# Kernel optimization log

Measured on AMD Instinct MI355X. Metric: run time of the kernel, lower is better.

## Reference

```python
import jax, jax.numpy as jnp
import numpy as np

N_NODES = 100000
N_EDGES = 3200000
D_IN = 256
D_OUT = 256


def setup_inputs() -> dict:
    key = jax.random.key(0)
    k1, k2, k3, k4, k5, k6 = jax.random.split(key, 6)
    x = jax.random.normal(k1, (N_NODES, D_IN), dtype=jnp.float32)
    edge_row = jax.random.randint(k2, (N_EDGES,), 0, N_NODES, dtype=jnp.int32)
    edge_col = jax.random.randint(k3, (N_EDGES,), 0, N_NODES, dtype=jnp.int32)
    edge_val = jax.random.uniform(k4, (N_EDGES,), dtype=jnp.float32)
    # nn.Linear params (PyTorch stores weight as [out, in]; we apply x @ W.T + b)
    bound = 1.0 / np.sqrt(D_IN)
    W = jax.random.uniform(k5, (D_OUT, D_IN), minval=-bound, maxval=bound, dtype=jnp.float32)
    b = jax.random.uniform(k6, (D_OUT,), minval=-bound, maxval=bound, dtype=jnp.float32)
    return {"x": x, "edge_row": edge_row, "edge_col": edge_col,
            "edge_val": edge_val, "W": W, "b": b}


def reference(x, edge_row, edge_col, edge_val, W, b):
    # SpMM: agg[i] = sum over edges e with row[e]==i of val[e] * x[col[e]]
    messages = edge_val[:, None] * x[edge_col]          # [E, D_in]
    agg = jax.ops.segment_sum(messages, edge_row, num_segments=N_NODES)  # [N, D_in]
    # Dense linear: agg @ W.T + b
    return jnp.einsum('nd,od->no', agg, W) + b
```

## Files before the change

### kernel.cpp

```cpp
#include <hip/hip_runtime.h>

#define THREADS 256

typedef __attribute__((ext_vector_type(8))) short short8;
typedef __attribute__((ext_vector_type(4))) float f32x4;

__device__ __forceinline__ unsigned short f2bf(float f) {
    unsigned u = __builtin_bit_cast(unsigned, f);
    return (unsigned short)((u + 0x7FFFu + ((u >> 16) & 1u)) >> 16);
}
__device__ __forceinline__ float bf2f_lo(unsigned u) { return __builtin_bit_cast(float, u << 16); }
__device__ __forceinline__ float bf2f_hi(unsigned u) { return __builtin_bit_cast(float, u & 0xFFFF0000u); }


__global__ void init_gcur512(int* __restrict__ gcur, int capB) {
    int i = blockIdx.x * blockDim.x + threadIdx.x;
    if (i < 512) gcur[i] = i * capB;
}

__global__ void p1_sort(const int* __restrict__ row, const int* __restrict__ col,
                        const float* __restrict__ val, int* __restrict__ gcur,
                        uint2* __restrict__ estage, int n_edges, int nbkt, int capB) {
    __shared__ int h[512];
    __shared__ int curl[512];
    int tid = threadIdx.x, bid = blockIdx.x;
    int E0 = (int)((long long)bid * n_edges / gridDim.x);
    int E1 = (int)((long long)(bid + 1) * n_edges / gridDim.x);
    for (int i = tid; i < 512; i += THREADS) h[i] = 0;
    __syncthreads();
    for (int e = E0 + tid; e < E1; e += THREADS)
        atomicAdd(&h[row[e] >> 8], 1);
    __syncthreads();
    for (int b = tid; b < nbkt; b += THREADS) {
        int c = h[b];
        curl[b] = c ? atomicAdd(&gcur[b], c) : 0;
    }
    __syncthreads();
    for (int e = E0 + tid; e < E1; e += THREADS) {
        int r = row[e];
        int b = r >> 8;
        int pos = atomicAdd(&curl[b], 1);
        if (pos < (b + 1) * capB)
            estage[pos] = make_uint2(((unsigned)(r & 255) << 24) | (unsigned)col[e],
                                     (unsigned)__float_as_int(val[e]));
    }
}

__global__ void bcnt_kernel(const int* __restrict__ gcur, int* __restrict__ bcnt,
                            int capB, int nbkt) {
    int i = blockIdx.x * blockDim.x + threadIdx.x;
    if (i < nbkt) {
        int c = gcur[i] - i * capB;
        bcnt[i] = c > capB ? capB : c;
    }
}

__global__ void bscan_kernel(const int* __restrict__ cnt, int* __restrict__ offs,
                             int* __restrict__ cur, int n) {
    __shared__ int buf[2][THREADS];
    __shared__ int running_s;
    int tid = threadIdx.x;
    if (tid == 0) running_s = 0;
    __syncthreads();
    for (int base = 0; base < n; base += THREADS) {
        int idx = base + tid;
        int v = (idx < n) ? cnt[idx] : 0;
        int incl = v;
        int cb = 0;
        buf[0][tid] = incl;
        __syncthreads();
        #pragma unroll
        for (int off = 1; off < THREADS; off <<= 1) {
            int t = incl;
            if (tid >= off) t += buf[cb][tid - off];
            cb ^= 1;
            buf[cb][tid] = t;
            incl = t;
            __syncthreads();
        }
        int base_run = running_s;
        if (idx < n) {
            int excl = base_run + incl - v;
            offs[idx] = excl;
            cur[idx] = excl;
        }
        int total = buf[cb][THREADS - 1];
        __syncthreads();
        if (tid == 0) running_s = base_run + total;
        __syncthreads();
    }
    if (tid == 0) offs[n] = running_s;
}

__global__ void p2_sort(const uint2* __restrict__ estage, const int* __restrict__ gcur,
                        const int* __restrict__ bbase, int2* __restrict__ pr,
                        int* __restrict__ offs, int capB, int n_nodes, int n_edges,
                        int nbkt) {
    __shared__ int h[256];
    __shared__ int curh[256];
    __shared__ int wsum[4];
    int b = blockIdx.x, tid = threadIdx.x;
    int base = b * capB;
    int count = gcur[b] - base; if (count > capB) count = capB;
    h[tid] = 0;
    __syncthreads();
    for (int i = tid; i < count; i += THREADS)
        atomicAdd(&h[estage[base + i].x >> 24], 1);
    __syncthreads();
    int v = h[tid];
    int lane = tid & 63, w = tid >> 6;
    int incl = v;
    #pragma unroll
    for (int off = 1; off < 64; off <<= 1) {
        int t = __shfl_up(incl, off, 64);
        if (lane >= off) incl += t;
    }
    if (lane == 63) wsum[w] = incl;
    __syncthreads();
    int wo = 0;
    for (int i = 0; i < w; ++i) wo += wsum[i];
    int excl = wo + incl - v;
    int gb = bbase[b];
    int node = b * 256 + tid;
    if (node < n_nodes) offs[node] = gb + excl;
    curh[tid] = gb + excl;
    if (b == nbkt - 1 && tid == 0) offs[n_nodes] = n_edges;
    __syncthreads();
    for (int i = tid; i < count; i += THREADS) {
        uint2 p = estage[base + i];
        int q = atomicAdd(&curh[(int)(p.x >> 24)], 1);
        pr[q] = make_int2((int)(p.x & 0x00FFFFFFu), (int)p.y);
    }
}


__global__ void zero_kernel(int* __restrict__ p, int n) {
    int i = blockIdx.x * blockDim.x + threadIdx.x;
    if (i < n) p[i] = 0;
}

__global__ void hist_part_kernel(const int* __restrict__ row, int* __restrict__ cnt,
                                 int n_edges, int n_nodes) {
    int g = blockIdx.x & 7;
    int inst = blockIdx.x >> 3;
    int ninst = gridDim.x >> 3;
    int lo = (int)(((long long)g * n_nodes) >> 3);
    int hi = (int)(((long long)(g + 1) * n_nodes) >> 3);
    int e0 = (int)(((long long)inst * n_edges) / ninst);
    int e1 = (int)(((long long)(inst + 1) * n_edges) / ninst);
    for (int e = e0 + threadIdx.x; e < e1; e += THREADS) {
        int r = row[e];
        if (r >= lo && r < hi) atomicAdd(&cnt[r], 1);
    }
}

__global__ void place_part_kernel(const int* __restrict__ row, const int* __restrict__ col,
                                  const float* __restrict__ val, int* __restrict__ cur,
                                  int2* __restrict__ pr, int n_edges, int n_nodes) {
    int g = blockIdx.x & 7;
    int inst = blockIdx.x >> 3;
    int ninst = gridDim.x >> 3;
    int lo = (int)(((long long)g * n_nodes) >> 3);
    int hi = (int)(((long long)(g + 1) * n_nodes) >> 3);
    int e0 = (int)(((long long)inst * n_edges) / ninst);
    int e1 = (int)(((long long)(inst + 1) * n_edges) / ninst);
    for (int e = e0 + threadIdx.x; e < e1; e += THREADS) {
        int r = row[e];
        if (r >= lo && r < hi) {
            int p = atomicAdd(&cur[r], 1);
            pr[p] = make_int2(col[e], __float_as_int(val[e]));
        }
    }
}

__global__ void scan1_kernel(const int* __restrict__ cnt, int* __restrict__ offs,
                             int* __restrict__ bsum, int n) {
    int tid = threadIdx.x;
    int base = blockIdx.x * 1024 + tid * 4;
    int v0 = 0, v1 = 0, v2 = 0, v3 = 0;
    if (base + 3 < n) {
        int4 v = *reinterpret_cast<const int4*>(cnt + base);
        v0 = v.x; v1 = v.y; v2 = v.z; v3 = v.w;
    } else {
        if (base + 0 < n) v0 = cnt[base + 0];
        if (base + 1 < n) v1 = cnt[base + 1];
        if (base + 2 < n) v2 = cnt[base + 2];
    }
    int ts = v0 + v1 + v2 + v3;
    int lane = tid & 63;
    int incl = ts;
    #pragma unroll
    for (int off = 1; off < 64; off <<= 1) {
        int t = __shfl_up(incl, off, 64);
        if (lane >= off) incl += t;
    }
    __shared__ int wsum[4];
    int w = tid >> 6;
    if (lane == 63) wsum[w] = incl;
    __syncthreads();
    int wo = 0;
    for (int i = 0; i < w; ++i) wo += wsum[i];
    int excl = wo + incl - ts;
    if (base + 0 < n) offs[base + 0] = excl;
    if (base + 1 < n) offs[base + 1] = excl + v0;
    if (base + 2 < n) offs[base + 2] = excl + v0 + v1;
    if (base + 3 < n) offs[base + 3] = excl + v0 + v1 + v2;
    if (tid == THREADS - 1) bsum[blockIdx.x] = wo + incl;
}

__global__ void scan2_kernel(int* __restrict__ bsum, int nb) {
    int tid = threadIdx.x;
    int base = tid * 4;
    int v0 = 0, v1 = 0, v2 = 0, v3 = 0;
    if (base + 0 < nb) v0 = bsum[base + 0];
    if (base + 1 < nb) v1 = bsum[base + 1];
    if (base + 2 < nb) v2 = bsum[base + 2];
    if (base + 3 < nb) v3 = bsum[base + 3];
    int ts = v0 + v1 + v2 + v3;
    int lane = tid & 63;
    int incl = ts;
    #pragma unroll
    for (int off = 1; off < 64; off <<= 1) {
        int t = __shfl_up(incl, off, 64);
        if (lane >= off) incl += t;
    }
    __shared__ int wsum[4];
    int w = tid >> 6;
    if (lane == 63) wsum[w] = incl;
    __syncthreads();
    int wo = 0;
    for (int i = 0; i < w; ++i) wo += wsum[i];
    int excl = wo + incl - ts;
    if (base + 0 < nb) bsum[base + 0] = excl;
    if (base + 1 < nb) bsum[base + 1] = excl + v0;
    if (base + 2 < nb) bsum[base + 2] = excl + v0 + v1;
    if (base + 3 < nb) bsum[base + 3] = excl + v0 + v1 + v2;
    if (tid == THREADS - 1) bsum[nb] = wo + incl;
}

__global__ void scan3_kernel(int* __restrict__ offs, const int* __restrict__ bsum,
                             int* __restrict__ cur, int n) {
    int i = blockIdx.x * blockDim.x + threadIdx.x;
    if (i < n) {
        int v = offs[i] + bsum[i >> 10];
        offs[i] = v;
        cur[i] = v;
    }
    if (i == 0) offs[n] = bsum[(n + 1023) >> 10];
}


__global__ void cvt_bf16_kernel(const float4* __restrict__ in, uint4* __restrict__ out, int n8) {
    int i = blockIdx.x * blockDim.x + threadIdx.x;
    if (i >= n8) return;
    float4 a = in[2 * i], b = in[2 * i + 1];
    uint4 o;
    o.x = (unsigned)f2bf(a.x) | ((unsigned)f2bf(a.y) << 16);
    o.y = (unsigned)f2bf(a.z) | ((unsigned)f2bf(a.w) << 16);
    o.z = (unsigned)f2bf(b.x) | ((unsigned)f2bf(b.y) << 16);
    o.w = (unsigned)f2bf(b.z) | ((unsigned)f2bf(b.w) << 16);
    out[i] = o;
}

__global__ void cvt_W_pack_kernel(const float* __restrict__ W, unsigned short* __restrict__ WbP) {
    int f = blockIdx.x * blockDim.x + threadIdx.x;
    if (f >= 8192) return;
    int l = f & 63, nt = (f >> 6) & 15, k0i = f >> 10;
    int r = nt * 16 + (l & 15);
    int koff = k0i * 32 + 8 * (l >> 4);
    const float4* s = reinterpret_cast<const float4*>(W + r * 256 + koff);
    float4 a = s[0], b = s[1];
    uint4 o;
    o.x = (unsigned)f2bf(a.x) | ((unsigned)f2bf(a.y) << 16);
    o.y = (unsigned)f2bf(a.z) | ((unsigned)f2bf(a.w) << 16);
    o.z = (unsigned)f2bf(b.x) | ((unsigned)f2bf(b.y) << 16);
    o.w = (unsigned)f2bf(b.z) | ((unsigned)f2bf(b.w) << 16);
    reinterpret_cast<uint4*>(WbP)[f] = o;
}

template<int OUT_BF16>
__global__ void spmm_bf16_kernel(const uint2* __restrict__ xb, const int* __restrict__ offs,
                                 const int2* __restrict__ pr, void* __restrict__ outp,
                                 int nnodes) {
    int wid = (blockIdx.x * blockDim.x + threadIdx.x) >> 6;
    int lane = threadIdx.x & 63;
    if (wid >= nnodes) return;
    int s = offs[wid], e = offs[wid + 1];
    float a0 = 0.f, a1 = 0.f, a2 = 0.f, a3 = 0.f;
    int i = s;
    if (i < e && (i & 1)) {
        int2 p = pr[i];
        uint2 xv = xb[(size_t)p.x * 64 + lane];
        float v = __int_as_float(p.y);
        a0 = fmaf(v, bf2f_lo(xv.x), a0); a1 = fmaf(v, bf2f_hi(xv.x), a1);
        a2 = fmaf(v, bf2f_lo(xv.y), a2); a3 = fmaf(v, bf2f_hi(xv.y), a3);
        ++i;
    }
    for (; i + 8 <= e; i += 8) {
        int4 pa = *reinterpret_cast<const int4*>(pr + i);
        int4 pb = *reinterpret_cast<const int4*>(pr + i + 2);
        int4 pc = *reinterpret_cast<const int4*>(pr + i + 4);
        int4 pd = *reinterpret_cast<const int4*>(pr + i + 6);
        uint2 x0 = xb[(size_t)pa.x * 64 + lane];
        uint2 x1 = xb[(size_t)pa.z * 64 + lane];
        uint2 x2 = xb[(size_t)pb.x * 64 + lane];
        uint2 x3 = xb[(size_t)pb.z * 64 + lane];
        uint2 x4_ = xb[(size_t)pc.x * 64 + lane];
        uint2 x5 = xb[(size_t)pc.z * 64 + lane];
        uint2 x6 = xb[(size_t)pd.x * 64 + lane];
        uint2 x7 = xb[(size_t)pd.z * 64 + lane];
        float v0 = __int_as_float(pa.y), v1 = __int_as_float(pa.w);
        float v2 = __int_as_float(pb.y), v3 = __int_as_float(pb.w);
        float v4 = __int_as_float(pc.y), v5 = __int_as_float(pc.w);
        float v6 = __int_as_float(pd.y), v7 = __int_as_float(pd.w);
        a0 = fmaf(v0, bf2f_lo(x0.x), a0); a1 = fmaf(v0, bf2f_hi(x0.x), a1);
        a2 = fmaf(v0, bf2f_lo(x0.y), a2); a3 = fmaf(v0, bf2f_hi(x0.y), a3);
        a0 = fmaf(v1, bf2f_lo(x1.x), a0); a1 = fmaf(v1, bf2f_hi(x1.x), a1);
        a2 = fmaf(v1, bf2f_lo(x1.y), a2); a3 = fmaf(v1, bf2f_hi(x1.y), a3);
        a0 = fmaf(v2, bf2f_lo(x2.x), a0); a1 = fmaf(v2, bf2f_hi(x2.x), a1);
        a2 = fmaf(v2, bf2f_lo(x2.y), a2); a3 = fmaf(v2, bf2f_hi(x2.y), a3);
        a0 = fmaf(v3, bf2f_lo(x3.x), a0); a1 = fmaf(v3, bf2f_hi(x3.x), a1);
        a2 = fmaf(v3, bf2f_lo(x3.y), a2); a3 = fmaf(v3, bf2f_hi(x3.y), a3);
        a0 = fmaf(v4, bf2f_lo(x4_.x), a0); a1 = fmaf(v4, bf2f_hi(x4_.x), a1);
        a2 = fmaf(v4, bf2f_lo(x4_.y), a2); a3 = fmaf(v4, bf2f_hi(x4_.y), a3);
        a0 = fmaf(v5, bf2f_lo(x5.x), a0); a1 = fmaf(v5, bf2f_hi(x5.x), a1);
        a2 = fmaf(v5, bf2f_lo(x5.y), a2); a3 = fmaf(v5, bf2f_hi(x5.y), a3);
        a0 = fmaf(v6, bf2f_lo(x6.x), a0); a1 = fmaf(v6, bf2f_hi(x6.x), a1);
        a2 = fmaf(v6, bf2f_lo(x6.y), a2); a3 = fmaf(v6, bf2f_hi(x6.y), a3);
        a0 = fmaf(v7, bf2f_lo(x7.x), a0); a1 = fmaf(v7, bf2f_hi(x7.x), a1);
        a2 = fmaf(v7, bf2f_lo(x7.y), a2); a3 = fmaf(v7, bf2f_hi(x7.y), a3);
    }
    for (; i + 2 <= e; i += 2) {
        int4 pa = *reinterpret_cast<const int4*>(pr + i);
        uint2 x0 = xb[(size_t)pa.x * 64 + lane];
        uint2 x1 = xb[(size_t)pa.z * 64 + lane];
        float v0 = __int_as_float(pa.y), v1 = __int_as_float(pa.w);
        a0 = fmaf(v0, bf2f_lo(x0.x), a0); a1 = fmaf(v0, bf2f_hi(x0.x), a1);
        a2 = fmaf(v0, bf2f_lo(x0.y), a2); a3 = fmaf(v0, bf2f_hi(x0.y), a3);
        a0 = fmaf(v1, bf2f_lo(x1.x), a0); a1 = fmaf(v1, bf2f_hi(x1.x), a1);
        a2 = fmaf(v1, bf2f_lo(x1.y), a2); a3 = fmaf(v1, bf2f_hi(x1.y), a3);
    }
    for (; i < e; ++i) {
        int2 p = pr[i];
        uint2 xv = xb[(size_t)p.x * 64 + lane];
        float v = __int_as_float(p.y);
        a0 = fmaf(v, bf2f_lo(xv.x), a0); a1 = fmaf(v, bf2f_hi(xv.x), a1);
        a2 = fmaf(v, bf2f_lo(xv.y), a2); a3 = fmaf(v, bf2f_hi(xv.y), a3);
    }
    if (OUT_BF16) {
        ushort4 o;
        o.x = f2bf(a0); o.y = f2bf(a1); o.z = f2bf(a2); o.w = f2bf(a3);
        *reinterpret_cast<ushort4*>((unsigned short*)outp + (size_t)wid * 256 + 4 * lane) = o;
    } else {
        ((float4*)outp)[(size_t)wid * 64 + lane] = make_float4(a0, a1, a2, a3);
    }
}

__global__ void spmm_f32_kernel(const float4* __restrict__ x4, const int* __restrict__ offs,
                                const int2* __restrict__ pr, float4* __restrict__ out4,
                                int nnodes) {
    int wid = (blockIdx.x * blockDim.x + threadIdx.x) >> 6;
    int lane = threadIdx.x & 63;
    if (wid >= nnodes) return;
    int s = offs[wid], e = offs[wid + 1];
    float4 acc = make_float4(0.f, 0.f, 0.f, 0.f);
    for (int i = s; i < e; ++i) {
        int2 p = pr[i];
        float4 xv = x4[(size_t)p.x * 64 + lane];
        float v = __int_as_float(p.y);
        acc.x = fmaf(v, xv.x, acc.x); acc.y = fmaf(v, xv.y, acc.y);
        acc.z = fmaf(v, xv.z, acc.z); acc.w = fmaf(v, xv.w, acc.w);
    }
    out4[(size_t)wid * 64 + lane] = acc;
}

__launch_bounds__(256)
__global__ void gemm_direct_kernel(const unsigned short* __restrict__ aggb,
                                   const unsigned short* __restrict__ WbP,
                                   const float* __restrict__ bias,
                                   float* __restrict__ out, int n) {
    int tid = threadIdx.x, lane = tid & 63, w = tid >> 6;
    int row0 = blockIdx.x * 64 + w * 16;
    int lr = lane & 15, lg = lane >> 4;
    const unsigned short* arow = aggb + (size_t)(row0 + lr) * 256 + lg * 8;
    short8 af[8];
    #pragma unroll
    for (int k = 0; k < 8; ++k)
        af[k] = *reinterpret_cast<const short8*>(arow + k * 32);
    f32x4 acc[16];
    #pragma unroll
    for (int nt = 0; nt < 16; ++nt) acc[nt] = (f32x4){0.f, 0.f, 0.f, 0.f};
    #pragma unroll
    for (int k = 0; k < 8; ++k) {
        #pragma unroll
        for (int nt = 0; nt < 16; ++nt) {
            short8 bf_ = *reinterpret_cast<const short8*>(
                &WbP[(size_t)((k * 16 + nt) * 64 + lane) * 8]);
            acc[nt] = __builtin_amdgcn_mfma_f32_16x16x32_bf16(af[k], bf_, acc[nt], 0, 0, 0);
        }
    }
    #pragma unroll
    for (int nt = 0; nt < 16; ++nt) {
        int gc = nt * 16 + lr;
        float bv = bias[gc];
        #pragma unroll
        for (int q = 0; q < 4; ++q) {
            int gr = row0 + lg * 4 + q;
            if (gr < n) out[(size_t)gr * 256 + gc] = acc[nt][q] + bv;
        }
    }
}

__launch_bounds__(256, 2)
__global__ void gemm_mfma_kernel(float* __restrict__ out, const unsigned short* __restrict__ Wb,
                                 const float* __restrict__ bias, int nrows) {
    __shared__ unsigned short As[64][264];
    __shared__ unsigned short Ws[256][40];
    int tid = threadIdx.x;
    int rowBase = blockIdx.x * 64;

    const float4* o4 = reinterpret_cast<const float4*>(out);
    for (int it = tid; it < 64 * 64; it += 256) {
        int r = it >> 6, c = it & 63;
        float4 v = make_float4(0.f, 0.f, 0.f, 0.f);
        int gr = rowBase + r;
        if (gr < nrows) v = o4[(size_t)gr * 64 + c];
        ushort4 w;
        w.x = f2bf(v.x); w.y = f2bf(v.y); w.z = f2bf(v.z); w.w = f2bf(v.w);
        *reinterpret_cast<ushort4*>(&As[r][c * 4]) = w;
    }

    int w = tid >> 6, lane = tid & 63;
    int lr = lane & 15, lg = lane >> 4;
    f32x4 acc[16];
    #pragma unroll
    for (int nt = 0; nt < 16; ++nt) acc[nt] = (f32x4){0.f, 0.f, 0.f, 0.f};

    for (int k0 = 0; k0 < 256; k0 += 32) {
        __syncthreads();
        for (int it = tid; it < 1024; it += 256) {
            int r = it >> 2, c = it & 3;
            uint4 v = *reinterpret_cast<const uint4*>(Wb + (size_t)r * 256 + k0 + c * 8);
            *reinterpret_cast<uint4*>(&Ws[r][c * 8]) = v;
        }
        __syncthreads();
        short8 af = *reinterpret_cast<const short8*>(&As[w * 16 + lr][k0 + 8 * lg]);
        #pragma unroll
        for (int nt = 0; nt < 16; ++nt) {
            short8 bf_ = *reinterpret_cast<const short8*>(&Ws[nt * 16 + lr][8 * lg]);
            acc[nt] = __builtin_amdgcn_mfma_f32_16x16x32_bf16(af, bf_, acc[nt], 0, 0, 0);
        }
    }

    #pragma unroll
    for (int nt = 0; nt < 16; ++nt) {
        int gc = nt * 16 + lr;
        float bv = bias[gc];
        #pragma unroll
        for (int q = 0; q < 4; ++q) {
            int gr = rowBase + w * 16 + lg * 4 + q;
            if (gr < nrows) out[(size_t)gr * 256 + gc] = acc[nt][q] + bv;
        }
    }
}


extern "C" void kernel_launch(void* const* d_in, const int* in_sizes, int n_in,
                              void* d_out, int out_size, void* d_ws, size_t ws_size,
                              hipStream_t stream) {
    const float* x     = (const float*)d_in[0];
    const int*   erow  = (const int*)d_in[1];
    const int*   ecol  = (const int*)d_in[2];
    const float* evalv = (const float*)d_in[3];
    const float* W     = (const float*)d_in[4];
    const float* bias  = (const float*)d_in[5];
    float* out = (float*)d_out;

    int n_nodes = in_sizes[0] / 256;
    int n_edges = in_sizes[1];

    int nbkt = (n_nodes + 255) >> 8;
    int avg = n_edges / (nbkt > 0 ? nbkt : 1);
    int capB = avg + avg / 4 + 1024;

    size_t A = (size_t)((n_nodes + 63) & ~63) + 64;
    int* offs  = (int*)d_ws;
    int* gcur  = offs + A;
    int* bcnt_ = gcur + 512;
    int* bbase = bcnt_ + 512;
    int* bscr  = bbase + 576;
    unsigned short* Wb  = (unsigned short*)(bscr + 512);
    unsigned short* WbP = Wb + 65536;
    int2* pr = (int2*)(WbP + 65536);
    int* after_pr = (int*)(pr + n_edges);

    size_t est_ints  = (size_t)nbkt * capB * 2;
    size_t aggb_ints = (size_t)n_nodes * 128;
    size_t xb_ints   = (size_t)n_nodes * 128;
    size_t alias_ints = est_ints > aggb_ints ? est_ints : aggb_ints;
    size_t head_ints = (size_t)(after_pr - (int*)d_ws);
    size_t need_new = (head_ints + alias_ints + xb_ints) * 4;
    bool new_ok = (nbkt <= 512) && (nbkt >= 1) && ws_size >= need_new;

    if (new_ok) {
        uint2* estage = (uint2*)after_pr;
        unsigned short* aggb = (unsigned short*)after_pr;
        unsigned short* xb = (unsigned short*)(after_pr + alias_ints);

        init_gcur512<<<2, THREADS, 0, stream>>>(gcur, capB);
        p1_sort<<<512, THREADS, 0, stream>>>(erow, ecol, evalv, gcur, estage,
                                             n_edges, nbkt, capB);
        bcnt_kernel<<<2, THREADS, 0, stream>>>(gcur, bcnt_, capB, nbkt);
        bscan_kernel<<<1, THREADS, 0, stream>>>(bcnt_, bbase, bscr, nbkt);
        p2_sort<<<nbkt, THREADS, 0, stream>>>(estage, gcur, bbase, pr, offs,
                                              capB, n_nodes, n_edges, nbkt);

        cvt_W_pack_kernel<<<32, THREADS, 0, stream>>>(W, WbP);
        int n8 = n_nodes * 32;
        cvt_bf16_kernel<<<(n8 + THREADS - 1) / THREADS, THREADS, 0, stream>>>(
            (const float4*)x, (uint4*)xb, n8);

        int spmm_blocks = (n_nodes + 3) / 4;
        spmm_bf16_kernel<1><<<spmm_blocks, THREADS, 0, stream>>>(
            (const uint2*)xb, offs, pr, aggb, n_nodes);
        int gb = (n_nodes + 63) / 64;
        gemm_direct_kernel<<<gb, THREADS, 0, stream>>>(aggb, WbP, bias, out, n_nodes);
    } else {
        int nb = (n_nodes + 1023) >> 10;
        size_t Af = (size_t)((n_nodes + 63) & ~63);
        int* cnt   = (int*)d_ws;
        int* offsf = cnt + Af;
        int* cur   = offsf + Af;
        int* bsum  = cur + Af;
        int* wbase = bsum + (((size_t)nb + 64) & ~63ull);
        unsigned short* Wbf = (unsigned short*)wbase;
        int2* prf  = (int2*)(Wbf + 65536);
        int* aft   = (int*)(prf + n_edges);
        unsigned short* xbf = (unsigned short*)aft;
        size_t need_old = (size_t)((char*)(xbf + (size_t)n_nodes * 256) - (char*)d_ws);
        bool told = ws_size >= need_old;

        zero_kernel<<<(n_nodes + THREADS - 1) / THREADS, THREADS, 0, stream>>>(cnt, n_nodes);
        hist_part_kernel<<<2048, THREADS, 0, stream>>>(erow, cnt, n_edges, n_nodes);
        scan1_kernel<<<nb, THREADS, 0, stream>>>(cnt, offsf, bsum, n_nodes);
        scan2_kernel<<<1, THREADS, 0, stream>>>(bsum, nb);
        scan3_kernel<<<(n_nodes + THREADS - 1) / THREADS, THREADS, 0, stream>>>(offsf, bsum, cur, n_nodes);
        place_part_kernel<<<2048, THREADS, 0, stream>>>(erow, ecol, evalv, cur, prf, n_edges, n_nodes);
        cvt_bf16_kernel<<<32, THREADS, 0, stream>>>((const float4*)W, (uint4*)Wbf, 65536 / 8);

        int gb = (n_nodes + 63) / 64;
        if (told) {
            int n8 = n_nodes * 32;
            cvt_bf16_kernel<<<(n8 + THREADS - 1) / THREADS, THREADS, 0, stream>>>(
                (const float4*)x, (uint4*)xbf, n8);
            int spmm_blocks = (n_nodes + 3) / 4;
            spmm_bf16_kernel<0><<<spmm_blocks, THREADS, 0, stream>>>(
                (const uint2*)xbf, offsf, prf, out, n_nodes);
        } else {
            int spmm_blocks = (n_nodes + 3) / 4;
            spmm_f32_kernel<<<spmm_blocks, THREADS, 0, stream>>>(
                (const float4*)x, offsf, prf, (float4*)out, n_nodes);
        }
        gemm_mfma_kernel<<<gb, THREADS, 0, stream>>>(out, Wbf, bias, n_nodes);
    }
}
```

Before: 439.5 us.

## Fuse bucket sort, W and x conversions into one launch; drop scan kernels; widen GEMM tile

Merges the first-pass bucket sort, the W bf16 packing and the x bf16 conversion into a single launch split by block index, and raises the sort-pass block count. The separate bucket-count and scan kernels are removed: gcur now holds relative counts, cleared by a memset, and each p2_sort block computes its own base offset by reducing the counts of earlier buckets. The GEMM now gives each wave 32 rows with two accumulator sets so that each loaded W fragment feeds two MFMAs. This trades several small serial launches for redundant per-block reductions and higher register pressure in the GEMM.

Result: slower. 455.6 us (+3.7%).

```diff
diff --git a/kernel.cpp b/kernel.cpp
--- a/kernel.cpp
+++ b/kernel.cpp
@@ -12,96 +12,89 @@
 __device__ __forceinline__ float bf2f_lo(unsigned u) { return __builtin_bit_cast(float, u << 16); }
 __device__ __forceinline__ float bf2f_hi(unsigned u) { return __builtin_bit_cast(float, u & 0xFFFF0000u); }
 
-
-__global__ void init_gcur512(int* __restrict__ gcur, int capB) {
-    int i = blockIdx.x * blockDim.x + threadIdx.x;
-    if (i < 512) gcur[i] = i * capB;
-}
-
-__global__ void p1_sort(const int* __restrict__ row, const int* __restrict__ col,
-                        const float* __restrict__ val, int* __restrict__ gcur,
-                        uint2* __restrict__ estage, int n_edges, int nbkt, int capB) {
-    __shared__ int h[512];
-    __shared__ int curl[512];
-    int tid = threadIdx.x, bid = blockIdx.x;
-    int E0 = (int)((long long)bid * n_edges / gridDim.x);
-    int E1 = (int)((long long)(bid + 1) * n_edges / gridDim.x);
-    for (int i = tid; i < 512; i += THREADS) h[i] = 0;
-    __syncthreads();
-    for (int e = E0 + tid; e < E1; e += THREADS)
-        atomicAdd(&h[row[e] >> 8], 1);
-    __syncthreads();
-    for (int b = tid; b < nbkt; b += THREADS) {
-        int c = h[b];
-        curl[b] = c ? atomicAdd(&gcur[b], c) : 0;
-    }
-    __syncthreads();
-    for (int e = E0 + tid; e < E1; e += THREADS) {
-        int r = row[e];
-        int b = r >> 8;
-        int pos = atomicAdd(&curl[b], 1);
-        if (pos < (b + 1) * capB)
-            estage[pos] = make_uint2(((unsigned)(r & 255) << 24) | (unsigned)col[e],
-                                     (unsigned)__float_as_int(val[e]));
-    }
-}
-
-__global__ void bcnt_kernel(const int* __restrict__ gcur, int* __restrict__ bcnt,
-                            int capB, int nbkt) {
-    int i = blockIdx.x * blockDim.x + threadIdx.x;
-    if (i < nbkt) {
-        int c = gcur[i] - i * capB;
-        bcnt[i] = c > capB ? capB : c;
-    }
-}
-
-__global__ void bscan_kernel(const int* __restrict__ cnt, int* __restrict__ offs,
-                             int* __restrict__ cur, int n) {
-    __shared__ int buf[2][THREADS];
-    __shared__ int running_s;
-    int tid = threadIdx.x;
-    if (tid == 0) running_s = 0;
-    __syncthreads();
-    for (int base = 0; base < n; base += THREADS) {
-        int idx = base + tid;
-        int v = (idx < n) ? cnt[idx] : 0;
-        int incl = v;
-        int cb = 0;
-        buf[0][tid] = incl;
+#define P1B 1024
+
+__global__ void fusedA_kernel(const int* __restrict__ row, const int* __restrict__ col,
+                              const float* __restrict__ val, int* __restrict__ gcur,
+                              uint2* __restrict__ estage,
+                              const float* __restrict__ W, unsigned short* __restrict__ WbP,
+                              const float4* __restrict__ x, uint4* __restrict__ xb,
+                              int n_edges, int nbkt, int capB, int n8) {
+    int b = blockIdx.x, tid = threadIdx.x;
+    if (b < P1B) {
+        __shared__ int h[512];
+        __shared__ int curl[512];
+        int E0 = (int)((long long)b * n_edges / P1B);
+        int E1 = (int)((long long)(b + 1) * n_edges / P1B);
+        for (int i = tid; i < 512; i += THREADS) h[i] = 0;
         __syncthreads();
-        #pragma unroll
-        for (int off = 1; off < THREADS; off <<= 1) {
-            int t = incl;
-            if (tid >= off) t += buf[cb][tid - off];
-            cb ^= 1;
-            buf[cb][tid] = t;
-            incl = t;
-            __syncthreads();
-        }
-        int base_run = running_s;
-        if (idx < n) {
-            int excl = base_run + incl - v;
-            offs[idx] = excl;
-            cur[idx] = excl;
-        }
-        int total = buf[cb][THREADS - 1];
+        for (int e = E0 + tid; e < E1; e += THREADS)
+            atomicAdd(&h[row[e] >> 8], 1);
         __syncthreads();
-        if (tid == 0) running_s = base_run + total;
+        for (int bk = tid; bk < nbkt; bk += THREADS) {
+            int c = h[bk];
+            curl[bk] = bk * capB + (c ? atomicAdd(&gcur[bk], c) : 0);
+        }
         __syncthreads();
-    }
-    if (tid == 0) offs[n] = running_s;
+        for (int e = E0 + tid; e < E1; e += THREADS) {
+            int r = row[e];
+            int bk = r >> 8;
+            int pos = atomicAdd(&curl[bk], 1);
+            if (pos < (bk + 1) * capB)
+                estage[pos] = make_uint2(((unsigned)(r & 255) << 24) | (unsigned)col[e],
+                                         (unsigned)__float_as_int(val[e]));
+        }
+    } else if (b < P1B + 32) {
+        int f = (b - P1B) * THREADS + tid;
+        int l = f & 63, nt = (f >> 6) & 15, k0i = f >> 10;
+        int r = nt * 16 + (l & 15);
+        int koff = k0i * 32 + 8 * (l >> 4);
+        const float4* s = reinterpret_cast<const float4*>(W + r * 256 + koff);
+        float4 a = s[0], bb = s[1];
+        uint4 o;
+        o.x = (unsigned)f2bf(a.x) | ((unsigned)f2bf(a.y) << 16);
+        o.y = (unsigned)f2bf(a.z) | ((unsigned)f2bf(a.w) << 16);
+        o.z = (unsigned)f2bf(bb.x) | ((unsigned)f2bf(bb.y) << 16);
+        o.w = (unsigned)f2bf(bb.z) | ((unsigned)f2bf(bb.w) << 16);
+        reinterpret_cast<uint4*>(WbP)[f] = o;
+    } else {
+        int i = (b - P1B - 32) * THREADS + tid;
+        if (i >= n8) return;
+        float4 a = x[2 * i], bb = x[2 * i + 1];
+        uint4 o;
+        o.x = (unsigned)f2bf(a.x) | ((unsigned)f2bf(a.y) << 16);
+        o.y = (unsigned)f2bf(a.z) | ((unsigned)f2bf(a.w) << 16);
+        o.z = (unsigned)f2bf(bb.x) | ((unsigned)f2bf(bb.y) << 16);
+        o.w = (unsigned)f2bf(bb.z) | ((unsigned)f2bf(bb.w) << 16);
+        reinterpret_cast<uint4*>(xb)[i] = o;
+    }
 }
 
 __global__ void p2_sort(const uint2* __restrict__ estage, const int* __restrict__ gcur,
-                        const int* __restrict__ bbase, int2* __restrict__ pr,
-                        int* __restrict__ offs, int capB, int n_nodes, int n_edges,
-                        int nbkt) {
+                        int2* __restrict__ pr, int* __restrict__ offs,
+                        int capB, int n_nodes, int nbkt) {
+    __shared__ int red[256];
     __shared__ int h[256];
     __shared__ int curh[256];
     __shared__ int wsum[4];
     int b = blockIdx.x, tid = threadIdx.x;
+
+    int partial = 0;
+    for (int j = tid; j < b; j += THREADS) {
+        int c = gcur[j];
+        partial += c > capB ? capB : c;
+    }
+    red[tid] = partial;
+    __syncthreads();
+    #pragma unroll
+    for (int s = 128; s > 0; s >>= 1) {
+        if (tid < s) red[tid] += red[tid + s];
+        __syncthreads();
+    }
+    int gb = red[0];
+    int count = gcur[b]; if (count > capB) count = capB;
     int base = b * capB;
-    int count = gcur[b] - base; if (count > capB) count = capB;
+
     h[tid] = 0;
     __syncthreads();
     for (int i = tid; i < count; i += THREADS)
@@ -120,162 +113,16 @@
     int wo = 0;
     for (int i = 0; i < w; ++i) wo += wsum[i];
     int excl = wo + incl - v;
-    int gb = bbase[b];
     int node = b * 256 + tid;
     if (node < n_nodes) offs[node] = gb + excl;
     curh[tid] = gb + excl;
-    if (b == nbkt - 1 && tid == 0) offs[n_nodes] = n_edges;
+    if (b == nbkt - 1 && tid == 0) offs[n_nodes] = gb + count;
     __syncthreads();
     for (int i = tid; i < count; i += THREADS) {
         uint2 p = estage[base + i];
         int q = atomicAdd(&curh[(int)(p.x >> 24)], 1);
         pr[q] = make_int2((int)(p.x & 0x00FFFFFFu), (int)p.y);
     }
-}
-
-
-__global__ void zero_kernel(int* __restrict__ p, int n) {
-    int i = blockIdx.x * blockDim.x + threadIdx.x;
-    if (i < n) p[i] = 0;
-}
-
-__global__ void hist_part_kernel(const int* __restrict__ row, int* __restrict__ cnt,
-                                 int n_edges, int n_nodes) {
-    int g = blockIdx.x & 7;
-    int inst = blockIdx.x >> 3;
-    int ninst = gridDim.x >> 3;
-    int lo = (int)(((long long)g * n_nodes) >> 3);
-    int hi = (int)(((long long)(g + 1) * n_nodes) >> 3);
-    int e0 = (int)(((long long)inst * n_edges) / ninst);
-    int e1 = (int)(((long long)(inst + 1) * n_edges) / ninst);
-    for (int e = e0 + threadIdx.x; e < e1; e += THREADS) {
-        int r = row[e];
-        if (r >= lo && r < hi) atomicAdd(&cnt[r], 1);
-    }
-}
-
-__global__ void place_part_kernel(const int* __restrict__ row, const int* __restrict__ col,
-                                  const float* __restrict__ val, int* __restrict__ cur,
-                                  int2* __restrict__ pr, int n_edges, int n_nodes) {
-    int g = blockIdx.x & 7;
-    int inst = blockIdx.x >> 3;
-    int ninst = gridDim.x >> 3;
-    int lo = (int)(((long long)g * n_nodes) >> 3);
-    int hi = (int)(((long long)(g + 1) * n_nodes) >> 3);
-    int e0 = (int)(((long long)inst * n_edges) / ninst);
-    int e1 = (int)(((long long)(inst + 1) * n_edges) / ninst);
-    for (int e = e0 + threadIdx.x; e < e1; e += THREADS) {
-        int r = row[e];
-        if (r >= lo && r < hi) {
-            int p = atomicAdd(&cur[r], 1);
-            pr[p] = make_int2(col[e], __float_as_int(val[e]));
-        }
-    }
-}
-
-__global__ void scan1_kernel(const int* __restrict__ cnt, int* __restrict__ offs,
-                             int* __restrict__ bsum, int n) {
-    int tid = threadIdx.x;
-    int base = blockIdx.x * 1024 + tid * 4;
-    int v0 = 0, v1 = 0, v2 = 0, v3 = 0;
-    if (base + 3 < n) {
-        int4 v = *reinterpret_cast<const int4*>(cnt + base);
-        v0 = v.x; v1 = v.y; v2 = v.z; v3 = v.w;
-    } else {
-        if (base + 0 < n) v0 = cnt[base + 0];
-        if (base + 1 < n) v1 = cnt[base + 1];
-        if (base + 2 < n) v2 = cnt[base + 2];
-    }
-    int ts = v0 + v1 + v2 + v3;
-    int lane = tid & 63;
-    int incl = ts;
-    #pragma unroll
-    for (int off = 1; off < 64; off <<= 1) {
-        int t = __shfl_up(incl, off, 64);
-        if (lane >= off) incl += t;
-    }
-    __shared__ int wsum[4];
-    int w = tid >> 6;
-    if (lane == 63) wsum[w] = incl;
-    __syncthreads();
-    int wo = 0;
-    for (int i = 0; i < w; ++i) wo += wsum[i];
-    int excl = wo + incl - ts;
-    if (base + 0 < n) offs[base + 0] = excl;
-    if (base + 1 < n) offs[base + 1] = excl + v0;
-    if (base + 2 < n) offs[base + 2] = excl + v0 + v1;
-    if (base + 3 < n) offs[base + 3] = excl + v0 + v1 + v2;
-    if (tid == THREADS - 1) bsum[blockIdx.x] = wo + incl;
-}
-
-__global__ void scan2_kernel(int* __restrict__ bsum, int nb) {
-    int tid = threadIdx.x;
-    int base = tid * 4;
-    int v0 = 0, v1 = 0, v2 = 0, v3 = 0;
-    if (base + 0 < nb) v0 = bsum[base + 0];
-    if (base + 1 < nb) v1 = bsum[base + 1];
-    if (base + 2 < nb) v2 = bsum[base + 2];
-    if (base + 3 < nb) v3 = bsum[base + 3];
-    int ts = v0 + v1 + v2 + v3;
-    int lane = tid & 63;
-    int incl = ts;
-    #pragma unroll
-    for (int off = 1; off < 64; off <<= 1) {
-        int t = __shfl_up(incl, off, 64);
-        if (lane >= off) incl += t;
-    }
-    __shared__ int wsum[4];
-    int w = tid >> 6;
-    if (lane == 63) wsum[w] = incl;
-    __syncthreads();
-    int wo = 0;
-    for (int i = 0; i < w; ++i) wo += wsum[i];
-    int excl = wo + incl - ts;
-    if (base + 0 < nb) bsum[base + 0] = excl;
-    if (base + 1 < nb) bsum[base + 1] = excl + v0;
-    if (base + 2 < nb) bsum[base + 2] = excl + v0 + v1;
-    if (base + 3 < nb) bsum[base + 3] = excl + v0 + v1 + v2;
-    if (tid == THREADS - 1) bsum[nb] = wo + incl;
-}
-
-__global__ void scan3_kernel(int* __restrict__ offs, const int* __restrict__ bsum,
-                             int* __restrict__ cur, int n) {
-    int i = blockIdx.x * blockDim.x + threadIdx.x;
-    if (i < n) {
-        int v = offs[i] + bsum[i >> 10];
-        offs[i] = v;
-        cur[i] = v;
-    }
-    if (i == 0) offs[n] = bsum[(n + 1023) >> 10];
-}
-
-
-__global__ void cvt_bf16_kernel(const float4* __restrict__ in, uint4* __restrict__ out, int n8) {
-    int i = blockIdx.x * blockDim.x + threadIdx.x;
-    if (i >= n8) return;
-    float4 a = in[2 * i], b = in[2 * i + 1];
-    uint4 o;
-    o.x = (unsigned)f2bf(a.x) | ((unsigned)f2bf(a.y) << 16);
-    o.y = (unsigned)f2bf(a.z) | ((unsigned)f2bf(a.w) << 16);
-    o.z = (unsigned)f2bf(b.x) | ((unsigned)f2bf(b.y) << 16);
-    o.w = (unsigned)f2bf(b.z) | ((unsigned)f2bf(b.w) << 16);
-    out[i] = o;
-}
-
-__global__ void cvt_W_pack_kernel(const float* __restrict__ W, unsigned short* __restrict__ WbP) {
-    int f = blockIdx.x * blockDim.x + threadIdx.x;
-    if (f >= 8192) return;
-    int l = f & 63, nt = (f >> 6) & 15, k0i = f >> 10;
-    int r = nt * 16 + (l & 15);
-    int koff = k0i * 32 + 8 * (l >> 4);
-    const float4* s = reinterpret_cast<const float4*>(W + r * 256 + koff);
-    float4 a = s[0], b = s[1];
-    uint4 o;
-    o.x = (unsigned)f2bf(a.x) | ((unsigned)f2bf(a.y) << 16);
-    o.y = (unsigned)f2bf(a.z) | ((unsigned)f2bf(a.w) << 16);
-    o.z = (unsigned)f2bf(b.x) | ((unsigned)f2bf(b.y) << 16);
-    o.w = (unsigned)f2bf(b.z) | ((unsigned)f2bf(b.w) << 16);
-    reinterpret_cast<uint4*>(WbP)[f] = o;
 }
 
 template<int OUT_BF16>
@@ -375,28 +222,31 @@
 }
 
 __launch_bounds__(256)
-__global__ void gemm_direct_kernel(const unsigned short* __restrict__ aggb,
-                                   const unsigned short* __restrict__ WbP,
-                                   const float* __restrict__ bias,
-                                   float* __restrict__ out, int n) {
+__global__ void gemm_direct2_kernel(const unsigned short* __restrict__ aggb,
+                                    const unsigned short* __restrict__ WbP,
+                                    const float* __restrict__ bias,
+                                    float* __restrict__ out, int n) {
     int tid = threadIdx.x, lane = tid & 63, w = tid >> 6;
-    int row0 = blockIdx.x * 64 + w * 16;
+    int row0 = blockIdx.x * 128 + w * 32;
     int lr = lane & 15, lg = lane >> 4;
-    const unsigned short* arow = aggb + (size_t)(row0 + lr) * 256 + lg * 8;
-    short8 af[8];
-    #pragma unroll
-    for (int k = 0; k < 8; ++k)
-        af[k] = *reinterpret_cast<const short8*>(arow + k * 32);
-    f32x4 acc[16];
-    #pragma unroll
-    for (int nt = 0; nt < 16; ++nt) acc[nt] = (f32x4){0.f, 0.f, 0.f, 0.f};
+    const unsigned short* arow0 = aggb + (size_t)(row0 + lr) * 256 + lg * 8;
+    const unsigned short* arow1 = arow0 + 16 * 256;
+    f32x4 acc0[16], acc1[16];
+    #pragma unroll
+    for (int nt = 0; nt < 16; ++nt) {
+        acc0[nt] = (f32x4){0.f, 0.f, 0.f, 0.f};
+        acc1[nt] = (f32x4){0.f, 0.f, 0.f, 0.f};
+    }
     #pragma unroll
     for (int k = 0; k < 8; ++k) {
+        short8 af0 = *reinterpret_cast<const short8*>(arow0 + k * 32);
+        short8 af1 = *reinterpret_cast<const short8*>(arow1 + k * 32);
         #pragma unroll
         for (int nt = 0; nt < 16; ++nt) {
             short8 bf_ = *reinterpret_cast<const short8*>(
                 &WbP[(size_t)((k * 16 + nt) * 64 + lane) * 8]);
-            acc[nt] = __builtin_amdgcn_mfma_f32_16x16x32_bf16(af[k], bf_, acc[nt], 0, 0, 0);
+            acc0[nt] = __builtin_amdgcn_mfma_f32_16x16x32_bf16(af0, bf_, acc0[nt], 0, 0, 0);
+            acc1[nt] = __builtin_amdgcn_mfma_f32_16x16x32_bf16(af1, bf_, acc1[nt], 0, 0, 0);
         }
     }
     #pragma unroll
@@ -405,10 +255,140 @@
         float bv = bias[gc];
         #pragma unroll
         for (int q = 0; q < 4; ++q) {
-            int gr = row0 + lg * 4 + q;
-            if (gr < n) out[(size_t)gr * 256 + gc] = acc[nt][q] + bv;
-        }
-    }
+            int gr0 = row0 + lg * 4 + q;
+            int gr1 = gr0 + 16;
+            if (gr0 < n) out[(size_t)gr0 * 256 + gc] = acc0[nt][q] + bv;
+            if (gr1 < n) out[(size_t)gr1 * 256 + gc] = acc1[nt][q] + bv;
+        }
+    }
+}
+
+
+__global__ void zero_kernel(int* __restrict__ p, int n) {
+    int i = blockIdx.x * blockDim.x + threadIdx.x;
+    if (i < n) p[i] = 0;
+}
+
+__global__ void hist_part_kernel(const int* __restrict__ row, int* __restrict__ cnt,
+                                 int n_edges, int n_nodes) {
+    int g = blockIdx.x & 7;
+    int inst = blockIdx.x >> 3;
+    int ninst = gridDim.x >> 3;
+    int lo = (int)(((long long)g * n_nodes) >> 3);
+    int hi = (int)(((long long)(g + 1) * n_nodes) >> 3);
+    int e0 = (int)(((long long)inst * n_edges) / ninst);
+    int e1 = (int)(((long long)(inst + 1) * n_edges) / ninst);
+    for (int e = e0 + threadIdx.x; e < e1; e += THREADS) {
+        int r = row[e];
+        if (r >= lo && r < hi) atomicAdd(&cnt[r], 1);
+    }
+}
+
+__global__ void place_part_kernel(const int* __restrict__ row, const int* __restrict__ col,
+                                  const float* __restrict__ val, int* __restrict__ cur,
+                                  int2* __restrict__ pr, int n_edges, int n_nodes) {
+    int g = blockIdx.x & 7;
+    int inst = blockIdx.x >> 3;
+    int ninst = gridDim.x >> 3;
+    int lo = (int)(((long long)g * n_nodes) >> 3);
+    int hi = (int)(((long long)(g + 1) * n_nodes) >> 3);
+    int e0 = (int)(((long long)inst * n_edges) / ninst);
+    int e1 = (int)(((long long)(inst + 1) * n_edges) / ninst);
+    for (int e = e0 + threadIdx.x; e < e1; e += THREADS) {
+        int r = row[e];
+        if (r >= lo && r < hi) {
+            int p = atomicAdd(&cur[r], 1);
+            pr[p] = make_int2(col[e], __float_as_int(val[e]));
+        }
+    }
+}
+
+__global__ void scan1_kernel(const int* __restrict__ cnt, int* __restrict__ offs,
+                             int* __restrict__ bsum, int n) {
+    int tid = threadIdx.x;
+    int base = blockIdx.x * 1024 + tid * 4;
+    int v0 = 0, v1 = 0, v2 = 0, v3 = 0;
+    if (base + 3 < n) {
+        int4 v = *reinterpret_cast<const int4*>(cnt + base);
+        v0 = v.x; v1 = v.y; v2 = v.z; v3 = v.w;
+    } else {
+        if (base + 0 < n) v0 = cnt[base + 0];
+        if (base + 1 < n) v1 = cnt[base + 1];
+        if (base + 2 < n) v2 = cnt[base + 2];
+    }
+    int ts = v0 + v1 + v2 + v3;
+    int lane = tid & 63;
+    int incl = ts;
+    #pragma unroll
+    for (int off = 1; off < 64; off <<= 1) {
+        int t = __shfl_up(incl, off, 64);
+        if (lane >= off) incl += t;
+    }
+    __shared__ int wsum[4];
+    int w = tid >> 6;
+    if (lane == 63) wsum[w] = incl;
+    __syncthreads();
+    int wo = 0;
+    for (int i = 0; i < w; ++i) wo += wsum[i];
+    int excl = wo + incl - ts;
+    if (base + 0 < n) offs[base + 0] = excl;
+    if (base + 1 < n) offs[base + 1] = excl + v0;
+    if (base + 2 < n) offs[base + 2] = excl + v0 + v1;
+    if (base + 3 < n) offs[base + 3] = excl + v0 + v1 + v2;
+    if (tid == THREADS - 1) bsum[blockIdx.x] = wo + incl;
+}
+
+__global__ void scan2_kernel(int* __restrict__ bsum, int nb) {
+    int tid = threadIdx.x;
+    int base = tid * 4;
+    int v0 = 0, v1 = 0, v2 = 0, v3 = 0;
+    if (base + 0 < nb) v0 = bsum[base + 0];
+    if (base + 1 < nb) v1 = bsum[base + 1];
+    if (base + 2 < nb) v2 = bsum[base + 2];
+    if (base + 3 < nb) v3 = bsum[base + 3];
+    int ts = v0 + v1 + v2 + v3;
+    int lane = tid & 63;
+    int incl = ts;
+    #pragma unroll
+    for (int off = 1; off < 64; off <<= 1) {
+        int t = __shfl_up(incl, off, 64);
+        if (lane >= off) incl += t;
+    }
+    __shared__ int wsum[4];
+    int w = tid >> 6;
+    if (lane == 63) wsum[w] = incl;
+    __syncthreads();
+    int wo = 0;
+    for (int i = 0; i < w; ++i) wo += wsum[i];
+    int excl = wo + incl - ts;
+    if (base + 0 < nb) bsum[base + 0] = excl;
+    if (base + 1 < nb) bsum[base + 1] = excl + v0;
+    if (base + 2 < nb) bsum[base + 2] = excl + v0 + v1;
+    if (base + 3 < nb) bsum[base + 3] = excl + v0 + v1 + v2;
+    if (tid == THREADS - 1) bsum[nb] = wo + incl;
+}
+
+__global__ void scan3_kernel(int* __restrict__ offs, const int* __restrict__ bsum,
+                             int* __restrict__ cur, int n) {
+    int i = blockIdx.x * blockDim.x + threadIdx.x;
+    if (i < n) {
+        int v = offs[i] + bsum[i >> 10];
+        offs[i] = v;
+        cur[i] = v;
+    }
+    if (i == 0) offs[n] = bsum[(n + 1023) >> 10];
+}
+
+__global__ void cvt_bf16_kernel(const float4* __restrict__ in, uint4* __restrict__ out, int n8) {
+    int i = blockIdx.x * blockDim.x + threadIdx.x;
+    if (i >= n8) return;
+    float4 a = in[2 * i], b = in[2 * i + 1];
+    uint4 o;
+    o.x = (unsigned)f2bf(a.x) | ((unsigned)f2bf(a.y) << 16);
+    o.y = (unsigned)f2bf(a.z) | ((unsigned)f2bf(a.w) << 16);
+    o.z = (unsigned)f2bf(b.x) | ((unsigned)f2bf(b.y) << 16);
+    o.w = (unsigned)f2bf(b.z) | ((unsigned)f2bf(b.w) << 16);
+    out[i] = o;
 }
 
 __launch_bounds__(256, 2)
@@ -486,45 +466,36 @@
     size_t A = (size_t)((n_nodes + 63) & ~63) + 64;
     int* offs  = (int*)d_ws;
     int* gcur  = offs + A;
-    int* bcnt_ = gcur + 512;
-    int* bbase = bcnt_ + 512;
-    int* bscr  = bbase + 576;
-    unsigned short* Wb  = (unsigned short*)(bscr + 512);
-    unsigned short* WbP = Wb + 65536;
+    unsigned short* WbP = (unsigned short*)(gcur + 512);
     int2* pr = (int2*)(WbP + 65536);
     int* after_pr = (int*)(pr + n_edges);
 
     size_t est_ints  = (size_t)nbkt * capB * 2;
-    size_t aggb_ints = (size_t)n_nodes * 128;
+    size_t aggb_ints = (size_t)n_nodes * 128 + 32768;
     size_t xb_ints   = (size_t)n_nodes * 128;
     size_t alias_ints = est_ints > aggb_ints ? est_ints : aggb_ints;
     size_t head_ints = (size_t)(after_pr - (int*)d_ws);
     size_t need_new = (head_ints + alias_ints + xb_ints) * 4;
-    bool new_ok = (nbkt <= 512) && (nbkt >= 1) && ws_size >= need_new;
+    bool new_ok = (nbkt <= 512) && (nbkt >= 1) && (n_nodes <= (1 << 24)) && ws_size >= need_new;
 
     if (new_ok) {
         uint2* estage = (uint2*)after_pr;
         unsigned short* aggb = (unsigned short*)after_pr;
         unsigned short* xb = (unsigned short*)(after_pr + alias_ints);
 
-        init_gcur512<<<2, THREADS, 0, stream>>>(gcur, capB);
-        p1_sort<<<512, THREADS, 0, stream>>>(erow, ecol, evalv, gcur, estage,
-                                             n_edges, nbkt, capB);
-        bcnt_kernel<<<2, THREADS, 0, stream>>>(gcur, bcnt_, capB, nbkt);
-        bscan_kernel<<<1, THREADS, 0, stream>>>(bcnt_, bbase, bscr, nbkt);
-        p2_sort<<<nbkt, THREADS, 0, stream>>>(estage, gcur, bbase, pr, offs,
-                                              capB, n_nodes, n_edges, nbkt);
-
-        cvt_W_pack_kernel<<<32, THREADS, 0, stream>>>(W, WbP);
+        hipMemsetAsync(gcur, 0, 512 * sizeof(int), stream);
         int n8 = n_nodes * 32;
-        cvt_bf16_kernel<<<(n8 + THREADS - 1) / THREADS, THREADS, 0, stream>>>(
-            (const float4*)x, (uint4*)xb, n8);
+        int cvtx_blocks = (n8 + THREADS - 1) / THREADS;
+        fusedA_kernel<<<P1B + 32 + cvtx_blocks, THREADS, 0, stream>>>(
+            erow, ecol, evalv, gcur, estage, W, WbP, (const float4*)x, (uint4*)xb,
+            n_edges, nbkt, capB, n8);
+        p2_sort<<<nbkt, THREADS, 0, stream>>>(estage, gcur, pr, offs, capB, n_nodes, nbkt);
 
         int spmm_blocks = (n_nodes + 3) / 4;
         spmm_bf16_kernel<1><<<spmm_blocks, THREADS, 0, stream>>>(
             (const uint2*)xb, offs, pr, aggb, n_nodes);
-        int gb = (n_nodes + 63) / 64;
-        gemm_direct_kernel<<<gb, THREADS, 0, stream>>>(aggb, WbP, bias, out, n_nodes);
+        int gb2 = (n_nodes + 127) / 128;
+        gemm_direct2_kernel<<<gb2, THREADS, 0, stream>>>(aggb, WbP, bias, out, n_nodes);
     } else {
         int nb = (n_nodes + 1023) >> 10;
         size_t Af = (size_t)((n_nodes + 63) & ~63);
```
